# Optimization experiments

Hardware: AMD Instinct MI355X
Metric: run time of the kernel (lower is better)

The kernel has to match this reference:

```python
import jax, jax.numpy as jnp
import numpy as np

DIM = 768
HEADS = 12
DIM_HEAD = 64
INNER = HEADS * DIM_HEAD  # 768
SCALE = DIM_HEAD ** -0.5


def setup_inputs() -> dict:
    key = jax.random.key(0)
    k1, k2, k3, k4 = jax.random.split(key, 4)
    b, n = 8, 1024
    x = jax.random.normal(k1, (b, n, DIM), dtype=jnp.float32)
    # fused QKV projection, no bias: y = x @ w_qkv  -> [b, n, 3*inner]
    w_qkv = jax.random.normal(k2, (DIM, 3 * INNER), dtype=jnp.float32) * (DIM ** -0.5)
    # output projection with bias
    w_out = jax.random.normal(k3, (INNER, DIM), dtype=jnp.float32) * (INNER ** -0.5)
    b_out = jax.random.normal(k4, (DIM,), dtype=jnp.float32) * 0.02
    return {"x": x, "w_qkv": w_qkv, "w_out": w_out, "b_out": b_out}


def reference(x, w_qkv, w_out, b_out):
    b, n, _ = x.shape
    qkv = jnp.einsum('bnd,de->bne', x, w_qkv)  # [b, n, 3*inner]
    q, k, v = jnp.split(qkv, 3, axis=-1)
    # 'b n (h d) -> b h n d'
    def split_heads(t):
        return t.reshape(b, n, HEADS, DIM_HEAD).transpose(0, 2, 1, 3)
    q, k, v = split_heads(q), split_heads(k), split_heads(v)
    dots = jnp.einsum('bhid,bhjd->bhij', q, k) * SCALE  # [b, h, n, n]
    attn = jax.nn.softmax(dots, axis=-1)
    out = jnp.einsum('bhij,bhjd->bhid', attn, v)  # [b, h, n, d]
    out = out.transpose(0, 2, 1, 3).reshape(b, n, INNER)  # 'b h n d -> b n (h d)'
    return jnp.einsum('bne,ed->bnd', out, w_out) + b_out
```

## Files before the change

kernel.cpp:

```cpp
#include <hip/hip_runtime.h>

typedef unsigned short u16;
typedef __bf16 bf16x8 __attribute__((ext_vector_type(8)));
typedef float f32x4 __attribute__((ext_vector_type(4)));

__device__ inline u16 f2bf(float f) {
    union { float f; unsigned int u; } a; a.f = f;
    unsigned int u = a.u + 0x7fffu + ((a.u >> 16) & 1u);
    return (u16)(u >> 16);
}

__device__ __forceinline__ void cp16(const void* g, void* l) {
    __builtin_amdgcn_global_load_lds(
        (const __attribute__((address_space(1))) unsigned int*)g,
        (__attribute__((address_space(3))) unsigned int*)l, 16, 0, 0);
}

__global__ __launch_bounds__(256) void prep(
    const float* __restrict__ x, const float* __restrict__ wq,
    const float* __restrict__ wo, u16* __restrict__ xbf,
    u16* __restrict__ wtq, u16* __restrict__ wto)
{
    int bid = blockIdx.x;
    if (bid < 3072) {
        size_t base = ((size_t)bid * 256 + threadIdx.x) * 8;
        float4 f0 = *(const float4*)&x[base];
        float4 f1 = *(const float4*)&x[base + 4];
        union { u16 s[8]; uint4 v; } t;
        t.s[0]=f2bf(f0.x); t.s[1]=f2bf(f0.y); t.s[2]=f2bf(f0.z); t.s[3]=f2bf(f0.w);
        t.s[4]=f2bf(f1.x); t.s[5]=f2bf(f1.y); t.s[6]=f2bf(f1.z); t.s[7]=f2bf(f1.w);
        *(uint4*)&xbf[base] = t.v;
        return;
    }
    __shared__ u16 tile[32][33];
    const float* in; u16* outp; int N, bx, by;
    if (bid < 3072 + 1728) { int t = bid - 3072; in = wq; outp = wtq; N = 2304; bx = t % 72; by = t / 72; }
    else                   { int t = bid - 4800; in = wo; outp = wto; N = 768;  bx = t % 24; by = t / 24; }
    int n0 = bx * 32, k0 = by * 32;
    int tx = threadIdx.x & 31, ty = threadIdx.x >> 5;
    #pragma unroll
    for (int r = ty; r < 32; r += 8)
        tile[r][tx] = f2bf(in[(size_t)(k0 + r) * N + n0 + tx]);
    __syncthreads();
    #pragma unroll
    for (int r = ty; r < 32; r += 8)
        outp[(size_t)(n0 + r) * 768 + k0 + tx] = tile[tx][r];
}

__global__ __launch_bounds__(256) void gemm_qkv(
    const u16* __restrict__ A, const u16* __restrict__ Bt,
    u16* __restrict__ q_out, u16* __restrict__ k_out, u16* __restrict__ v_out)
{
    const int K = 768;
    __shared__ __align__(16) u16 As[2][128 * 64];
    __shared__ __align__(16) u16 Bs[2][128 * 64];

    int tid = threadIdx.x;
    int lane = tid & 63, wave = tid >> 6;
    int quad = lane >> 4, l16 = lane & 15;
    int wm = wave >> 1, wn = wave & 1;
    int id = blockIdx.x;
    int xcd = id & 7, j = id >> 3;
    int m0 = (((j & 7) << 3) + xcd) * 128;
    int n0 = (j >> 3) * 128;

    f32x4 acc[4][4];
    #pragma unroll
    for (int i = 0; i < 4; i++)
        #pragma unroll
        for (int jj = 0; jj < 4; jj++) acc[i][jj] = (f32x4){0.f, 0.f, 0.f, 0.f};

    int r0 = tid >> 3, cg = tid & 7;
    int g = cg ^ (r0 & 7);
    const u16* GA[4]; const u16* GB[4];
    #pragma unroll
    for (int it = 0; it < 4; it++) {
        GA[it] = A  + (size_t)(m0 + it * 32 + r0) * K + g * 8;
        GB[it] = Bt + (size_t)(n0 + it * 32 + r0) * K + g * 8;
    }

    #define STAGE_QKV(kt, b)                                          \
        _Pragma("unroll")                                             \
        for (int it = 0; it < 4; it++) {                              \
            cp16(GA[it] + (kt), &As[b][(it * 256 + tid) * 8]);        \
            cp16(GB[it] + (kt), &Bs[b][(it * 256 + tid) * 8]);        \
        }

    STAGE_QKV(0, 0)
    for (int i = 0; i < 12; i++) {
        int b = i & 1;
        if (i + 1 < 12) {
            STAGE_QKV((i + 1) * 64, b ^ 1)
            asm volatile("s_waitcnt vmcnt(8)" ::: "memory");
        } else {
            asm volatile("s_waitcnt vmcnt(0)" ::: "memory");
        }
        __builtin_amdgcn_s_barrier();
        bf16x8 af[2][4], bfr[2][4];
        #pragma unroll
        for (int ko = 0; ko < 2; ko++)
            #pragma unroll
            for (int x = 0; x < 4; x++) {
                int Ra = wm * 64 + x * 16 + l16;
                af[ko][x]  = *(const bf16x8*)&As[b][Ra * 64 + (((ko * 4 + quad) ^ (Ra & 7)) * 8)];
                int Rb = wn * 64 + x * 16 + l16;
                bfr[ko][x] = *(const bf16x8*)&Bs[b][Rb * 64 + (((ko * 4 + quad) ^ (Rb & 7)) * 8)];
            }
        #pragma unroll
        for (int ko = 0; ko < 2; ko++)
            #pragma unroll
            for (int x = 0; x < 4; x++)
                #pragma unroll
                for (int y = 0; y < 4; y++)
                    acc[x][y] = __builtin_amdgcn_mfma_f32_16x16x32_bf16(af[ko][x], bfr[ko][y], acc[x][y], 0, 0, 0);
        __builtin_amdgcn_s_barrier();
    }
    #undef STAGE_QKV

    int M0 = m0 + wm * 64, N0 = n0 + wn * 64;
    int part = N0 >= 1536 ? 2 : (N0 >= 768 ? 1 : 0);
    int h = (N0 - part * 768) >> 6;
    int b2 = M0 >> 10, npos0 = M0 & 1023;
    u16* ep = (wave < 2 ? As[0] : Bs[0]) + (wave & 1) * 4096;

    if (part != 2) {
        float scale = (part == 0) ? 0.18033688011112042f : 1.0f;
        u16* gbase = (part == 0 ? q_out : k_out) + (((size_t)(b2 * 12 + h) * 1024 + npos0) << 6);
        #pragma unroll
        for (int i = 0; i < 4; i++)
            #pragma unroll
            for (int jj = 0; jj < 4; jj++) {
                int dd = jj * 16 + l16;
                #pragma unroll
                for (int r = 0; r < 4; r++) {
                    int np = i * 16 + quad * 4 + r;
                    ep[np * 64 + (((dd >> 3) ^ (np & 7)) * 8) + (dd & 7)] =
                        f2bf(acc[i][jj][r] * scale);
                }
            }
        #pragma unroll
        for (int t = 0; t < 8; t++) {
            int idx = t * 512 + lane * 8;
            int np = idx >> 6;
            int slot = ((lane & 7) ^ (np & 7));
            uint4 v = *(const uint4*)&ep[np * 64 + slot * 8];
            *(uint4*)&gbase[idx] = v;
        }
    } else {
        #pragma unroll
        for (int i = 0; i < 4; i++)
            #pragma unroll
            for (int jj = 0; jj < 4; jj++) {
                int dd = jj * 16 + l16;
                int npg = i * 2 + (quad >> 1);
                int sub = (quad & 1) * 4;
                union { u16 s[4]; uint2 v; } pk;
                #pragma unroll
                for (int r = 0; r < 4; r++) pk.s[r] = f2bf(acc[i][jj][r]);
                *(uint2*)&ep[dd * 64 + ((npg ^ (dd & 7)) * 8) + sub] = pk.v;
            }
        #pragma unroll
        for (int t = 0; t < 8; t++) {
            int dd = t * 8 + (lane >> 3);
            int npg = lane & 7;
            uint4 v = *(const uint4*)&ep[dd * 64 + ((npg ^ (dd & 7)) * 8)];
            *(uint4*)&v_out[((size_t)((b2 * 12 + h) * 64 + dd)) * 1024 + npos0 + npg * 8] = v;
        }
    }
}

__global__ __launch_bounds__(512, 6) void attn128(
    u16* __restrict__ QO, const u16* __restrict__ Kg, const u16* __restrict__ Vtg)
{
    __shared__ __align__(16) u16 Ks[2][64 * 64];
    __shared__ __align__(16) u16 Vs[2][64 * 64];

    int tid = threadIdx.x;
    int lane = tid & 63, wave = tid >> 6;
    int quad = lane >> 4, l16 = lane & 15;
    int id = blockIdx.x;
    int xcd = id & 7, j = id >> 3;
    int bh = xcd * 12 + (j >> 3);
    int q0 = (j & 7) * 128;
    const size_t head_base = (size_t)bh * 65536;

    size_t qoff = head_base + (size_t)(q0 + wave * 16 + l16) * 64;
    bf16x8 qf0 = *(const bf16x8*)&QO[qoff + quad * 8];
    bf16x8 qf1 = *(const bf16x8*)&QO[qoff + 32 + quad * 8];

    f32x4 Oacc[4];
    #pragma unroll
    for (int dt = 0; dt < 4; dt++) Oacc[dt] = (f32x4){0.f, 0.f, 0.f, 0.f};
    f32x4 lacc = (f32x4){0.f, 0.f, 0.f, 0.f};

    union { unsigned int w[4]; bf16x8 v; } ones;
    ones.w[0] = ones.w[1] = ones.w[2] = ones.w[3] = 0x3f803f80u;

    int srow = tid >> 3, sg = tid & 7;
    int gsK = sg ^ (srow & 7);
    const u16* GK = Kg + head_base + (size_t)srow * 64 + gsK * 8;
    const u16* GV = Vtg + head_base + (size_t)srow * 1024 + sg * 8;
    const int vwA = srow * 64 + (((2 * sg)     ^ (srow & 15)) * 4);
    const int vwB = srow * 64 + (((2 * sg + 1) ^ (srow & 15)) * 4);

    uint4 vA, vB;
    {
        uint4 t0 = *(const uint4*)GV;
        uint2 t;
        t.x = t0.x; t.y = t0.y; *(uint2*)&Vs[0][vwA] = t;
        t.x = t0.z; t.y = t0.w; *(uint2*)&Vs[0][vwB] = t;
    }
    vA = *(const uint4*)(GV + 64);
    cp16(GK, &Ks[0][tid * 8]);

    #define ATT_STEP(I, DO_K, DO_LD, VLD, DO_WR, VWR)                            \
    {                                                                            \
        const int b = (I) & 1;                                                   \
        asm volatile("s_waitcnt vmcnt(0)" ::: "memory");                         \
        asm volatile("s_waitcnt lgkmcnt(0)" ::: "memory");                       \
        __builtin_amdgcn_s_barrier();                                            \
        if (DO_K) cp16(GK + (size_t)((I) + 1) * 4096, &Ks[b ^ 1][tid * 8]);      \
        if (DO_LD) VLD = *(const uint4*)(GV + ((I) + 2) * 64);                   \
        if (DO_WR) {                                                             \
            uint2 t;                                                             \
            t.x = VWR.x; t.y = VWR.y; *(uint2*)&Vs[b ^ 1][vwA] = t;              \
            t.x = VWR.z; t.y = VWR.w; *(uint2*)&Vs[b ^ 1][vwB] = t;              \
        }                                                                        \
        f32x4 s4[4];                                                             \
        _Pragma("unroll")                                                        \
        for (int nt = 0; nt < 4; nt++) {                                         \
            int R = nt * 16 + l16;                                               \
            bf16x8 kf0 = *(const bf16x8*)&Ks[b][R * 64 + ((quad       ^ (R & 7)) * 8)]; \
            bf16x8 kf1 = *(const bf16x8*)&Ks[b][R * 64 + (((quad + 4) ^ (R & 7)) * 8)]; \
            f32x4 s = (f32x4){0.f, 0.f, 0.f, 0.f};                               \
            s = __builtin_amdgcn_mfma_f32_16x16x32_bf16(kf0, qf0, s, 0, 0, 0);   \
            s = __builtin_amdgcn_mfma_f32_16x16x32_bf16(kf1, qf1, s, 0, 0, 0);   \
            s4[nt] = s;                                                          \
        }                                                                        \
        float p[4][4];                                                           \
        _Pragma("unroll")                                                        \
        for (int nt = 0; nt < 4; nt++)                                           \
            _Pragma("unroll")                                                    \
            for (int r = 0; r < 4; r++)                                          \
                p[nt][r] = __builtin_amdgcn_exp2f(s4[nt][r]);                    \
        __builtin_amdgcn_s_setprio(1);                                           \
        _Pragma("unroll")                                                        \
        for (int h = 0; h < 2; h++) {                                            \
            union { unsigned int w[4]; bf16x8 v; } pk;                           \
            asm("v_cvt_pk_bf16_f32 %0, %1, %2" : "=v"(pk.w[0]) : "v"(p[2*h][0]),   "v"(p[2*h][1]));   \
            asm("v_cvt_pk_bf16_f32 %0, %1, %2" : "=v"(pk.w[1]) : "v"(p[2*h][2]),   "v"(p[2*h][3]));   \
            asm("v_cvt_pk_bf16_f32 %0, %1, %2" : "=v"(pk.w[2]) : "v"(p[2*h+1][0]), "v"(p[2*h+1][1])); \
            asm("v_cvt_pk_bf16_f32 %0, %1, %2" : "=v"(pk.w[3]) : "v"(p[2*h+1][2]), "v"(p[2*h+1][3])); \
            lacc = __builtin_amdgcn_mfma_f32_16x16x32_bf16(ones.v, pk.v, lacc, 0, 0, 0); \
            int pbase = ((8 * h + quad) ^ l16) * 4;                              \
            _Pragma("unroll")                                                    \
            for (int dt = 0; dt < 4; dt++) {                                     \
                int drow = dt * 16 + l16;                                        \
                union { u16 s[8]; bf16x8 v; } vk;                                \
                *(uint2*)&vk.s[0] = *(const uint2*)&Vs[b][drow * 64 + pbase];    \
                *(uint2*)&vk.s[4] = *(const uint2*)&Vs[b][drow * 64 + (pbase ^ 16)]; \
                Oacc[dt] = __builtin_amdgcn_mfma_f32_16x16x32_bf16(vk.v, pk.v, Oacc[dt], 0, 0, 0); \
            }                                                                    \
        }                                                                        \
        __builtin_amdgcn_s_setprio(0);                                           \
    }

    for (int ii = 0; ii < 7; ii++) {
        ATT_STEP(2 * ii,     1, 1, vB, 1, vA)
        ATT_STEP(2 * ii + 1, 1, 1, vA, 1, vB)
    }
    ATT_STEP(14, 1, 0, vB, 1, vA)
    ATT_STEP(15, 0, 0, vA, 0, vB)
    #undef ATT_STEP

    {
        float rl = __builtin_amdgcn_rcpf(lacc[0]);
        #pragma unroll
        for (int dt = 0; dt < 4; dt++) {
            union { u16 s[4]; uint2 v; } ok;
            #pragma unroll
            for (int r = 0; r < 4; r++) ok.s[r] = f2bf(Oacc[dt][r] * rl);
            *(uint2*)&QO[qoff + dt * 16 + quad * 4] = ok.v;
        }
    }
}

__global__ __launch_bounds__(256) void gemm_out(
    const u16* __restrict__ Qg, const u16* __restrict__ Bt,
    const float* __restrict__ bias, float* __restrict__ out)
{
    const int K = 768;
    __shared__ __align__(16) u16 As[2][128 * 64];
    __shared__ __align__(16) u16 Bs[2][64 * 64];

    int tid = threadIdx.x;
    int lane = tid & 63, wave = tid >> 6;
    int quad = lane >> 4, l16 = lane & 15;
    int wm = wave >> 1, wn = wave & 1;
    int id = blockIdx.x;
    int xcd = id & 7, j = id >> 3;
    int m0 = (((j & 7) << 3) + xcd) * 128;
    int n0 = (j >> 3) * 64;

    f32x4 acc[4][2];
    #pragma unroll
    for (int i = 0; i < 4; i++)
        #pragma unroll
        for (int jj = 0; jj < 2; jj++) acc[i][jj] = (f32x4){0.f, 0.f, 0.f, 0.f};

    int r0 = tid >> 3, cg = tid & 7;
    int g = cg ^ (r0 & 7);
    const u16* GA[4]; const u16* GB[2];
    #pragma unroll
    for (int it = 0; it < 4; it++) {
        int m = m0 + it * 32 + r0, b = m >> 10, npos = m & 1023;
        GA[it] = Qg + (((size_t)(b * 12) * 1024 + npos) << 6) + g * 8;
    }
    #pragma unroll
    for (int it = 0; it < 2; it++)
        GB[it] = Bt + (size_t)(n0 + it * 32 + r0) * K + g * 8;

    #define STAGE_OUT(i2, b)                                              \
        _Pragma("unroll")                                                 \
        for (int it = 0; it < 4; it++)                                    \
            cp16(GA[it] + (size_t)(i2) * 65536, &As[b][(it * 256 + tid) * 8]); \
        _Pragma("unroll")                                                 \
        for (int it = 0; it < 2; it++)                                    \
            cp16(GB[it] + (i2) * 64,            &Bs[b][(it * 256 + tid) * 8]);

    STAGE_OUT(0, 0)
    for (int i = 0; i < 12; i++) {
        int b = i & 1;
        if (i + 1 < 12) {
            STAGE_OUT(i + 1, b ^ 1)
            asm volatile("s_waitcnt vmcnt(6)" ::: "memory");
        } else {
            asm volatile("s_waitcnt vmcnt(0)" ::: "memory");
        }
        __builtin_amdgcn_s_barrier();
        bf16x8 af[2][4], bfr[2][2];
        #pragma unroll
        for (int ko = 0; ko < 2; ko++) {
            #pragma unroll
            for (int x = 0; x < 4; x++) {
                int Ra = wm * 64 + x * 16 + l16;
                af[ko][x]  = *(const bf16x8*)&As[b][Ra * 64 + (((ko * 4 + quad) ^ (Ra & 7)) * 8)];
            }
            #pragma unroll
            for (int y = 0; y < 2; y++) {
                int Rb = wn * 32 + y * 16 + l16;
                bfr[ko][y] = *(const bf16x8*)&Bs[b][Rb * 64 + (((ko * 4 + quad) ^ (Rb & 7)) * 8)];
            }
        }
        #pragma unroll
        for (int ko = 0; ko < 2; ko++)
            #pragma unroll
            for (int x = 0; x < 4; x++)
                #pragma unroll
                for (int y = 0; y < 2; y++)
                    acc[x][y] = __builtin_amdgcn_mfma_f32_16x16x32_bf16(af[ko][x], bfr[ko][y], acc[x][y], 0, 0, 0);
        __builtin_amdgcn_s_barrier();
    }
    #undef STAGE_OUT

    #pragma unroll
    for (int i = 0; i < 4; i++) {
        int mbase = m0 + wm * 64 + i * 16 + quad * 4;
        #pragma unroll
        for (int jj = 0; jj < 2; jj++) {
            int n = n0 + wn * 32 + jj * 16 + l16;
            float bv = bias[n];
            #pragma unroll
            for (int r = 0; r < 4; r++)
                out[(size_t)(mbase + r) * 768 + n] = acc[i][jj][r] + bv;
        }
    }
}

extern "C" void kernel_launch(void* const* d_in, const int* in_sizes, int n_in,
                              void* d_out, int out_size, void* d_ws, size_t ws_size,
                              hipStream_t stream) {
    const float* x     = (const float*)d_in[0];
    const float* w_qkv = (const float*)d_in[1];
    const float* w_out = (const float*)d_in[2];
    const float* b_out = (const float*)d_in[3];
    float* out = (float*)d_out;

    char* ws = (char*)d_ws;
    u16* wtq  = (u16*)(ws);
    u16* wto  = (u16*)(ws + 3538944);
    u16* Qbuf = (u16*)(ws + 4718592);
    u16* xbf  = (u16*)(ws + 17301504);
    u16* Kbuf = (u16*)d_out;
    u16* Vbuf = (u16*)d_out + 6291456;

    prep<<<dim3(5376), 256, 0, stream>>>(x, w_qkv, w_out, xbf, wtq, wto);
    gemm_qkv<<<dim3(1152), 256, 0, stream>>>(xbf, wtq, Qbuf, Kbuf, Vbuf);
    attn128<<<dim3(768), 512, 0, stream>>>(Qbuf, Kbuf, Vbuf);
    gemm_out<<<dim3(768), 256, 0, stream>>>(Qbuf, wto, b_out, out);
}
```

Measured before the change: 172.8 us.

## Drop double buffering in QKV and output GEMMs, pack transpose stores

Replaces the double-buffered LDS prefetch pipeline in both GEMM kernels with a single buffer that loads, waits fully, then computes each K step. This halves LDS use per block, which may let more blocks run per CU, but it removes the overlap of global loads with MFMA work. It also widens the weight-transpose stores in the prep kernel to 32-bit packed pairs.

```diff
diff --git a/kernel.cpp b/kernel.cpp
--- a/kernel.cpp
+++ b/kernel.cpp
@@ -42,9 +42,14 @@
     for (int r = ty; r < 32; r += 8)
         tile[r][tx] = f2bf(in[(size_t)(k0 + r) * N + n0 + tx]);
     __syncthreads();
-    #pragma unroll
-    for (int r = ty; r < 32; r += 8)
-        outp[(size_t)(n0 + r) * 768 + k0 + tx] = tile[tx][r];
+    int tx2 = threadIdx.x & 15, ty2 = threadIdx.x >> 4;
+    #pragma unroll
+    for (int r = ty2; r < 32; r += 16) {
+        union { u16 s[2]; unsigned int v; } pk;
+        pk.s[0] = tile[2 * tx2][r];
+        pk.s[1] = tile[2 * tx2 + 1][r];
+        *(unsigned int*)&outp[(size_t)(n0 + r) * 768 + k0 + 2 * tx2] = pk.v;
+    }
 }
 
 __global__ __launch_bounds__(256) void gemm_qkv(
@@ -52,8 +57,8 @@
     u16* __restrict__ q_out, u16* __restrict__ k_out, u16* __restrict__ v_out)
 {
     const int K = 768;
-    __shared__ __align__(16) u16 As[2][128 * 64];
-    __shared__ __align__(16) u16 Bs[2][128 * 64];
+    __shared__ __align__(16) u16 As[128 * 64];
+    __shared__ __align__(16) u16 Bs[128 * 64];
 
     int tid = threadIdx.x;
     int lane = tid & 63, wave = tid >> 6;
@@ -79,22 +84,13 @@
         GB[it] = Bt + (size_t)(n0 + it * 32 + r0) * K + g * 8;
     }
 
-    #define STAGE_QKV(kt, b)                                          \
-        _Pragma("unroll")                                             \
-        for (int it = 0; it < 4; it++) {                              \
-            cp16(GA[it] + (kt), &As[b][(it * 256 + tid) * 8]);        \
-            cp16(GB[it] + (kt), &Bs[b][(it * 256 + tid) * 8]);        \
-        }
-
-    STAGE_QKV(0, 0)
     for (int i = 0; i < 12; i++) {
-        int b = i & 1;
-        if (i + 1 < 12) {
-            STAGE_QKV((i + 1) * 64, b ^ 1)
-            asm volatile("s_waitcnt vmcnt(8)" ::: "memory");
-        } else {
-            asm volatile("s_waitcnt vmcnt(0)" ::: "memory");
-        }
+        #pragma unroll
+        for (int it = 0; it < 4; it++) {
+            cp16(GA[it] + i * 64, &As[(it * 256 + tid) * 8]);
+            cp16(GB[it] + i * 64, &Bs[(it * 256 + tid) * 8]);
+        }
+        asm volatile("s_waitcnt vmcnt(0)" ::: "memory");
         __builtin_amdgcn_s_barrier();
         bf16x8 af[2][4], bfr[2][4];
         #pragma unroll
@@ -102,9 +98,9 @@
             #pragma unroll
             for (int x = 0; x < 4; x++) {
                 int Ra = wm * 64 + x * 16 + l16;
-                af[ko][x]  = *(const bf16x8*)&As[b][Ra * 64 + (((ko * 4 + quad) ^ (Ra & 7)) * 8)];
+                af[ko][x]  = *(const bf16x8*)&As[Ra * 64 + (((ko * 4 + quad) ^ (Ra & 7)) * 8)];
                 int Rb = wn * 64 + x * 16 + l16;
-                bfr[ko][x] = *(const bf16x8*)&Bs[b][Rb * 64 + (((ko * 4 + quad) ^ (Rb & 7)) * 8)];
+                bfr[ko][x] = *(const bf16x8*)&Bs[Rb * 64 + (((ko * 4 + quad) ^ (Rb & 7)) * 8)];
             }
         #pragma unroll
         for (int ko = 0; ko < 2; ko++)
@@ -115,13 +111,12 @@
                     acc[x][y] = __builtin_amdgcn_mfma_f32_16x16x32_bf16(af[ko][x], bfr[ko][y], acc[x][y], 0, 0, 0);
         __builtin_amdgcn_s_barrier();
     }
-    #undef STAGE_QKV
 
     int M0 = m0 + wm * 64, N0 = n0 + wn * 64;
     int part = N0 >= 1536 ? 2 : (N0 >= 768 ? 1 : 0);
     int h = (N0 - part * 768) >> 6;
     int b2 = M0 >> 10, npos0 = M0 & 1023;
-    u16* ep = (wave < 2 ? As[0] : Bs[0]) + (wave & 1) * 4096;
+    u16* ep = (wave < 2 ? As : Bs) + (wave & 1) * 4096;
 
     if (part != 2) {
         float scale = (part == 0) ? 0.18033688011112042f : 1.0f;
@@ -290,8 +285,8 @@
     const float* __restrict__ bias, float* __restrict__ out)
 {
     const int K = 768;
-    __shared__ __align__(16) u16 As[2][128 * 64];
-    __shared__ __align__(16) u16 Bs[2][64 * 64];
+    __shared__ __align__(16) u16 As[128 * 64];
+    __shared__ __align__(16) u16 Bs[64 * 64];
 
     int tid = threadIdx.x;
     int lane = tid & 63, wave = tid >> 6;
@@ -320,23 +315,14 @@
     for (int it = 0; it < 2; it++)
         GB[it] = Bt + (size_t)(n0 + it * 32 + r0) * K + g * 8;
 
-    #define STAGE_OUT(i2, b)                                              \
-        _Pragma("unroll")                                                 \
-        for (int it = 0; it < 4; it++)                                    \
-            cp16(GA[it] + (size_t)(i2) * 65536, &As[b][(it * 256 + tid) * 8]); \
-        _Pragma("unroll")                                                 \
-        for (int it = 0; it < 2; it++)                                    \
-            cp16(GB[it] + (i2) * 64,            &Bs[b][(it * 256 + tid) * 8]);
-
-    STAGE_OUT(0, 0)
     for (int i = 0; i < 12; i++) {
-        int b = i & 1;
-        if (i + 1 < 12) {
-            STAGE_OUT(i + 1, b ^ 1)
-            asm volatile("s_waitcnt vmcnt(6)" ::: "memory");
-        } else {
-            asm volatile("s_waitcnt vmcnt(0)" ::: "memory");
-        }
+        #pragma unroll
+        for (int it = 0; it < 4; it++)
+            cp16(GA[it] + (size_t)i * 65536, &As[(it * 256 + tid) * 8]);
+        #pragma unroll
+        for (int it = 0; it < 2; it++)
+            cp16(GB[it] + i * 64,            &Bs[(it * 256 + tid) * 8]);
+        asm volatile("s_waitcnt vmcnt(0)" ::: "memory");
         __builtin_amdgcn_s_barrier();
         bf16x8 af[2][4], bfr[2][2];
         #pragma unroll
@@ -344,12 +330,12 @@
             #pragma unroll
             for (int x = 0; x < 4; x++) {
                 int Ra = wm * 64 + x * 16 + l16;
-                af[ko][x]  = *(const bf16x8*)&As[b][Ra * 64 + (((ko * 4 + quad) ^ (Ra & 7)) * 8)];
+                af[ko][x]  = *(const bf16x8*)&As[Ra * 64 + (((ko * 4 + quad) ^ (Ra & 7)) * 8)];
             }
             #pragma unroll
             for (int y = 0; y < 2; y++) {
                 int Rb = wn * 32 + y * 16 + l16;
-                bfr[ko][y] = *(const bf16x8*)&Bs[b][Rb * 64 + (((ko * 4 + quad) ^ (Rb & 7)) * 8)];
+                bfr[ko][y] = *(const bf16x8*)&Bs[Rb * 64 + (((ko * 4 + quad) ^ (Rb & 7)) * 8)];
             }
         }
         #pragma unroll
@@ -361,7 +347,6 @@
                     acc[x][y] = __builtin_amdgcn_mfma_f32_16x16x32_bf16(af[ko][x], bfr[ko][y], acc[x][y], 0, 0, 0);
         __builtin_amdgcn_s_barrier();
     }
-    #undef STAGE_OUT
 
     #pragma unroll
     for (int i = 0; i < 4; i++) {
```

Result: slower. 181.2 us (+4.9%).

## Fuse fp32-to-bf16 conversion of x into QKV GEMM A-tile loading

Applied to the files above, without the earlier changes.

Drops the separate x-to-bf16 pass from the prep kernel. The QKV GEMM now reads fp32 x directly into registers, converts it with packed bf16 conversion instructions and writes it to LDS, double-buffered in a restructured software pipeline. This removes a full write and re-read of the bf16 copy of x and shrinks the prep kernel. In exchange it doubles the global bytes read for A inside the GEMM, adds register pressure (launch bounds now request 2 blocks), and adds more waitcnt handling. The weight transpose store is also widened to 32-bit packed writes.

```diff
diff --git a/kernel.cpp b/kernel.cpp
--- a/kernel.cpp
+++ b/kernel.cpp
@@ -17,41 +17,34 @@
 }
 
 __global__ __launch_bounds__(256) void prep(
-    const float* __restrict__ x, const float* __restrict__ wq,
-    const float* __restrict__ wo, u16* __restrict__ xbf,
+    const float* __restrict__ wq, const float* __restrict__ wo,
     u16* __restrict__ wtq, u16* __restrict__ wto)
 {
     int bid = blockIdx.x;
-    if (bid < 3072) {
-        size_t base = ((size_t)bid * 256 + threadIdx.x) * 8;
-        float4 f0 = *(const float4*)&x[base];
-        float4 f1 = *(const float4*)&x[base + 4];
-        union { u16 s[8]; uint4 v; } t;
-        t.s[0]=f2bf(f0.x); t.s[1]=f2bf(f0.y); t.s[2]=f2bf(f0.z); t.s[3]=f2bf(f0.w);
-        t.s[4]=f2bf(f1.x); t.s[5]=f2bf(f1.y); t.s[6]=f2bf(f1.z); t.s[7]=f2bf(f1.w);
-        *(uint4*)&xbf[base] = t.v;
-        return;
-    }
     __shared__ u16 tile[32][33];
     const float* in; u16* outp; int N, bx, by;
-    if (bid < 3072 + 1728) { int t = bid - 3072; in = wq; outp = wtq; N = 2304; bx = t % 72; by = t / 72; }
-    else                   { int t = bid - 4800; in = wo; outp = wto; N = 768;  bx = t % 24; by = t / 24; }
+    if (bid < 1728) { in = wq; outp = wtq; N = 2304; bx = bid % 72; by = bid / 72; }
+    else            { int t = bid - 1728; in = wo; outp = wto; N = 768;  bx = t % 24; by = t / 24; }
     int n0 = bx * 32, k0 = by * 32;
     int tx = threadIdx.x & 31, ty = threadIdx.x >> 5;
     #pragma unroll
     for (int r = ty; r < 32; r += 8)
         tile[r][tx] = f2bf(in[(size_t)(k0 + r) * N + n0 + tx]);
     __syncthreads();
-    #pragma unroll
-    for (int r = ty; r < 32; r += 8)
-        outp[(size_t)(n0 + r) * 768 + k0 + tx] = tile[tx][r];
-}
-
-__global__ __launch_bounds__(256) void gemm_qkv(
-    const u16* __restrict__ A, const u16* __restrict__ Bt,
+    int tx2 = threadIdx.x & 15, ty2 = threadIdx.x >> 4;
+    #pragma unroll
+    for (int r = ty2; r < 32; r += 16) {
+        union { u16 s[2]; unsigned int v; } pk;
+        pk.s[0] = tile[2 * tx2][r];
+        pk.s[1] = tile[2 * tx2 + 1][r];
+        *(unsigned int*)&outp[(size_t)(n0 + r) * 768 + k0 + 2 * tx2] = pk.v;
+    }
+}
+
+__global__ __launch_bounds__(256, 2) void gemm_qkv(
+    const float* __restrict__ X, const u16* __restrict__ Bt,
     u16* __restrict__ q_out, u16* __restrict__ k_out, u16* __restrict__ v_out)
 {
-    const int K = 768;
     __shared__ __align__(16) u16 As[2][128 * 64];
     __shared__ __align__(16) u16 Bs[2][128 * 64];
 
@@ -72,50 +65,100 @@
 
     int r0 = tid >> 3, cg = tid & 7;
     int g = cg ^ (r0 & 7);
-    const u16* GA[4]; const u16* GB[4];
+    const float* GX[4]; const u16* GB[4];
     #pragma unroll
     for (int it = 0; it < 4; it++) {
-        GA[it] = A  + (size_t)(m0 + it * 32 + r0) * K + g * 8;
-        GB[it] = Bt + (size_t)(n0 + it * 32 + r0) * K + g * 8;
-    }
-
-    #define STAGE_QKV(kt, b)                                          \
-        _Pragma("unroll")                                             \
-        for (int it = 0; it < 4; it++) {                              \
-            cp16(GA[it] + (kt), &As[b][(it * 256 + tid) * 8]);        \
-            cp16(GB[it] + (kt), &Bs[b][(it * 256 + tid) * 8]);        \
-        }
-
-    STAGE_QKV(0, 0)
-    for (int i = 0; i < 12; i++) {
-        int b = i & 1;
-        if (i + 1 < 12) {
-            STAGE_QKV((i + 1) * 64, b ^ 1)
-            asm volatile("s_waitcnt vmcnt(8)" ::: "memory");
-        } else {
-            asm volatile("s_waitcnt vmcnt(0)" ::: "memory");
-        }
-        __builtin_amdgcn_s_barrier();
-        bf16x8 af[2][4], bfr[2][4];
-        #pragma unroll
-        for (int ko = 0; ko < 2; ko++)
-            #pragma unroll
-            for (int x = 0; x < 4; x++) {
-                int Ra = wm * 64 + x * 16 + l16;
-                af[ko][x]  = *(const bf16x8*)&As[b][Ra * 64 + (((ko * 4 + quad) ^ (Ra & 7)) * 8)];
-                int Rb = wn * 64 + x * 16 + l16;
-                bfr[ko][x] = *(const bf16x8*)&Bs[b][Rb * 64 + (((ko * 4 + quad) ^ (Rb & 7)) * 8)];
-            }
-        #pragma unroll
-        for (int ko = 0; ko < 2; ko++)
-            #pragma unroll
-            for (int x = 0; x < 4; x++)
-                #pragma unroll
-                for (int y = 0; y < 4; y++)
-                    acc[x][y] = __builtin_amdgcn_mfma_f32_16x16x32_bf16(af[ko][x], bfr[ko][y], acc[x][y], 0, 0, 0);
-        __builtin_amdgcn_s_barrier();
-    }
-    #undef STAGE_QKV
+        GX[it] = X  + (size_t)(m0 + it * 32 + r0) * 768 + g * 8;
+        GB[it] = Bt + (size_t)(n0 + it * 32 + r0) * 768 + g * 8;
+    }
+
+    float4 aX[4][2], aY[4][2];
+
+    #define LOAD_A(SET, kt)                                       \
+        _Pragma("unroll")                                         \
+        for (int it = 0; it < 4; it++) {                          \
+            SET[it][0] = *(const float4*)(GX[it] + (kt));         \
+            SET[it][1] = *(const float4*)(GX[it] + (kt) + 4);     \
+        }
+    #define STAGE_B(kt, b)                                        \
+        _Pragma("unroll")                                         \
+        for (int it = 0; it < 4; it++)                            \
+            cp16(GB[it] + (kt), &Bs[b][(it * 256 + tid) * 8]);
+    #define WRITE_A(SET, b)                                       \
+        _Pragma("unroll")                                         \
+        for (int it = 0; it < 4; it++) {                          \
+            union { unsigned int w[4]; uint4 v; } pk;             \
+            asm("v_cvt_pk_bf16_f32 %0, %1, %2" : "=v"(pk.w[0]) : "v"(SET[it][0].x), "v"(SET[it][0].y)); \
+            asm("v_cvt_pk_bf16_f32 %0, %1, %2" : "=v"(pk.w[1]) : "v"(SET[it][0].z), "v"(SET[it][0].w)); \
+            asm("v_cvt_pk_bf16_f32 %0, %1, %2" : "=v"(pk.w[2]) : "v"(SET[it][1].x), "v"(SET[it][1].y)); \
+            asm("v_cvt_pk_bf16_f32 %0, %1, %2" : "=v"(pk.w[3]) : "v"(SET[it][1].z), "v"(SET[it][1].w)); \
+            *(uint4*)&As[b][(it * 256 + tid) * 8] = pk.v;         \
+        }
+    #define COMP(b)                                               \
+    {                                                             \
+        bf16x8 af[2][4], bfr[2][4];                               \
+        _Pragma("unroll")                                         \
+        for (int ko = 0; ko < 2; ko++)                            \
+            _Pragma("unroll")                                     \
+            for (int x = 0; x < 4; x++) {                         \
+                int Ra = wm * 64 + x * 16 + l16;                  \
+                af[ko][x]  = *(const bf16x8*)&As[b][Ra * 64 + (((ko * 4 + quad) ^ (Ra & 7)) * 8)]; \
+                int Rb = wn * 64 + x * 16 + l16;                  \
+                bfr[ko][x] = *(const bf16x8*)&Bs[b][Rb * 64 + (((ko * 4 + quad) ^ (Rb & 7)) * 8)]; \
+            }                                                     \
+        _Pragma("unroll")                                         \
+        for (int ko = 0; ko < 2; ko++)                            \
+            _Pragma("unroll")                                     \
+            for (int x = 0; x < 4; x++)                           \
+                _Pragma("unroll")                                 \
+                for (int y = 0; y < 4; y++)                       \
+                    acc[x][y] = __builtin_amdgcn_mfma_f32_16x16x32_bf16(af[ko][x], bfr[ko][y], acc[x][y], 0, 0, 0); \
+    }
+
+    LOAD_A(aX, 0)
+    LOAD_A(aY, 64)
+    STAGE_B(0, 0)
+    asm volatile("s_waitcnt vmcnt(12)" ::: "memory");
+    WRITE_A(aX, 0)
+
+    for (int ii = 0; ii < 5; ii++) {
+        int i0 = 2 * ii;
+        LOAD_A(aX, (i0 + 2) * 64)
+        STAGE_B((i0 + 1) * 64, 1)
+        asm volatile("s_waitcnt vmcnt(12)" ::: "memory");
+        WRITE_A(aY, 1)
+        asm volatile("s_waitcnt lgkmcnt(0)" ::: "memory");
+        __builtin_amdgcn_s_barrier();
+        COMP(0)
+        __builtin_amdgcn_s_barrier();
+
+        int i1 = i0 + 1;
+        LOAD_A(aY, (i1 + 2) * 64)
+        STAGE_B((i1 + 1) * 64, 0)
+        asm volatile("s_waitcnt vmcnt(12)" ::: "memory");
+        WRITE_A(aX, 0)
+        asm volatile("s_waitcnt lgkmcnt(0)" ::: "memory");
+        __builtin_amdgcn_s_barrier();
+        COMP(1)
+        __builtin_amdgcn_s_barrier();
+    }
+    STAGE_B(11 * 64, 1)
+    asm volatile("s_waitcnt vmcnt(4)" ::: "memory");
+    WRITE_A(aY, 1)
+    asm volatile("s_waitcnt lgkmcnt(0)" ::: "memory");
+    __builtin_amdgcn_s_barrier();
+    COMP(0)
+    __builtin_amdgcn_s_barrier();
+    asm volatile("s_waitcnt vmcnt(0)" ::: "memory");
+    asm volatile("s_waitcnt lgkmcnt(0)" ::: "memory");
+    __builtin_amdgcn_s_barrier();
+    COMP(1)
+    __builtin_amdgcn_s_barrier();
+
+    #undef LOAD_A
+    #undef STAGE_B
+    #undef WRITE_A
+    #undef COMP
 
     int M0 = m0 + wm * 64, N0 = n0 + wn * 64;
     int part = N0 >= 1536 ? 2 : (N0 >= 768 ? 1 : 0);
@@ -390,12 +433,11 @@
     u16* wtq  = (u16*)(ws);
     u16* wto  = (u16*)(ws + 3538944);
     u16* Qbuf = (u16*)(ws + 4718592);
-    u16* xbf  = (u16*)(ws + 17301504);
     u16* Kbuf = (u16*)d_out;
     u16* Vbuf = (u16*)d_out + 6291456;
 
-    prep<<<dim3(5376), 256, 0, stream>>>(x, w_qkv, w_out, xbf, wtq, wto);
-    gemm_qkv<<<dim3(1152), 256, 0, stream>>>(xbf, wtq, Qbuf, Kbuf, Vbuf);
+    prep<<<dim3(2304), 256, 0, stream>>>(w_qkv, w_out, wtq, wto);
+    gemm_qkv<<<dim3(1152), 256, 0, stream>>>(x, wtq, Qbuf, Kbuf, Vbuf);
     attn128<<<dim3(768), 512, 0, stream>>>(Qbuf, Kbuf, Vbuf);
     gemm_out<<<dim3(768), 256, 0, stream>>>(Qbuf, wto, b_out, out);
 }
```

After: 181.7 us. 5.1% more time.
